# Kernel optimization log

Hardware: AMD Instinct MI355X
Metric: run time of the kernel (lower is better)

The kernel has to match this reference:

```python
import jax, jax.numpy as jnp
import numpy as np

N_NODES = 50000
N_EDGES = 800000
IN_DIM = 128
HID = 128
TIME = 6.0
STEPS = 12


def setup_inputs() -> dict:
    key = jax.random.key(0)
    ks = jax.random.split(key, 8)
    gat_out = jax.random.normal(ks[0], (N_NODES, IN_DIM), dtype=jnp.float32)
    edge_index = jax.random.randint(ks[1], (2, N_EDGES), 0, N_NODES, dtype=jnp.int64)
    # scale weights like PyTorch Linear default (uniform-ish magnitude)
    W_in = jax.random.normal(ks[2], (IN_DIM, HID), dtype=jnp.float32) * (1.0 / np.sqrt(IN_DIM))
    b_in = jnp.zeros((HID,), dtype=jnp.float32)
    W1 = jax.random.normal(ks[3], (HID, 2 * HID), dtype=jnp.float32) * (1.0 / np.sqrt(HID))
    b1 = jnp.zeros((2 * HID,), dtype=jnp.float32)
    W2 = jax.random.normal(ks[4], (2 * HID, HID), dtype=jnp.float32) * (1.0 / np.sqrt(2 * HID))
    b2 = jnp.zeros((HID,), dtype=jnp.float32)
    clearance = jnp.full((1,), 0.1, dtype=jnp.float32)
    return {"gat_out": gat_out, "edge_index": edge_index, "W_in": W_in, "b_in": b_in,
            "W1": W1, "b1": b1, "W2": W2, "b2": b2, "clearance": clearance}


def reference(gat_out, edge_index, W_in, b_in, W1, b1, W2, b2, clearance):
    N = gat_out.shape[0]
    dt = TIME / STEPS
    src, dst = edge_index[0], edge_index[1]
    h = jnp.tanh(gat_out @ W_in + b_in)  # [N, HID]
    # degree is identical each Euler step in the original; hoist it once
    deg = jax.ops.segment_sum(jnp.ones((src.shape[0],), dtype=h.dtype), dst, num_segments=N)
    deg = jnp.clip(deg, 1.0, None)[:, None]  # [N, 1]
    decay = jax.nn.relu(clearance)  # [1]

    def step(h, _):
        agg = jax.ops.segment_sum(h[src], dst, num_segments=N) / deg  # [N, HID]
        diff = jnp.tanh(jax.nn.gelu(agg @ W1 + b1, approximate=False) @ W2 + b2)
        h = h + (diff - decay * h) * dt
        return h, None

    h, _ = jax.lax.scan(step, h, None, length=STEPS)
    return h
```

## Files before the change

kernel.cpp:

```cpp
#include <hip/hip_runtime.h>
#include <math.h>

#define N_NODES 50000
#define N_EDGES 800000
#define HID 128
#define H2 256
#define STEPS 12
#define DT 0.5f

#define NB ((N_NODES + 255) / 256)
#define NODE_BLOCKS ((N_NODES + 31) / 32)
#define N_PAD (NODE_BLOCKS * 32)
#define CSR_CAP (N_EDGES + 8 * N_NODES)

typedef __attribute__((ext_vector_type(8))) short bf16x8;
typedef __attribute__((ext_vector_type(4))) float f32x4;

__device__ inline unsigned short f2bf(float x) {
    unsigned int u = __float_as_uint(x);
    unsigned int r = (u + 0x7FFFu + ((u >> 16) & 1u)) >> 16;
    return (unsigned short)r;
}
__device__ inline float bf2f(unsigned short b) {
    return __uint_as_float(((unsigned int)b) << 16);
}
__device__ inline float u2f(unsigned int u) { return __uint_as_float(u); }

__device__ inline float fast_tanh(float x) {
    float xc = fminf(fmaxf(x, -9.0f), 9.0f);
    float t = __builtin_amdgcn_exp2f(xc * 2.8853900817779268f);
    return 1.0f - 2.0f * __builtin_amdgcn_rcpf(t + 1.0f);
}

__device__ inline float fast_gelu(float x) {
    float u  = x * 0.70710678118654752f;
    float au = fabsf(u);
    float t  = __builtin_amdgcn_rcpf(fmaf(0.3275911f, au, 1.0f));
    float poly = t * (0.254829592f + t * (-0.284496736f + t * (1.421413741f +
                 t * (-1.453152027f + t * 1.061405429f))));
    float ex = __builtin_amdgcn_exp2f(-au * au * 1.4426950408889634f);
    float erfv = copysignf(1.0f - poly * ex, u);
    return 0.5f * x * (1.0f + erfv);
}


__global__ void k_init(int* __restrict__ counts, int* __restrict__ gcur,
                       unsigned short* __restrict__ a, unsigned short* __restrict__ b,
                       const float* __restrict__ W1, const float* __restrict__ W2,
                       const float* __restrict__ Win,
                       unsigned short* __restrict__ w1h, unsigned short* __restrict__ w2h,
                       unsigned short* __restrict__ winh) {
    int i = blockIdx.x * 256 + threadIdx.x;
    if (i == 0) *gcur = 0;
    if (i < N_NODES) counts[i] = 0;
    if (i < (N_PAD - N_NODES) * HID) {
        a[(size_t)N_NODES * HID + i] = 0;
        b[(size_t)N_NODES * HID + i] = 0;
    }
    int tile = i >> 6, l = i & 63;
    if (tile < 160) {
        const float* W; unsigned short* out; int K, N, ti;
        if (tile < 64)       { W = W1;  out = w1h;  K = 128; N = 256; ti = tile; }
        else if (tile < 128) { W = W2;  out = w2h;  K = 256; N = 128; ti = tile - 64; }
        else                 { W = Win; out = winh; K = 128; N = 128; ti = tile - 128; }
        int KT = K >> 5;
        int kt = ti % KT, nt = ti / KT;
        int n  = nt * 16 + (l & 15);
        int k0 = kt * 32 + (l >> 4) * 8;
        int base = ((nt * KT + kt) * 64 + l) * 8;
        for (int j = 0; j < 8; j++)
            out[base + j] = f2bf(W[(size_t)(k0 + j) * N + n]);
    }
}

__global__ void k_hist(const int* __restrict__ dst, int* __restrict__ counts) {
    int e = blockIdx.x * 256 + threadIdx.x;
    if (e < N_EDGES) atomicAdd(&counts[dst[e]], 1);
}

__global__ void k_offsets_atomic(const int* __restrict__ counts, int* __restrict__ gcur,
                                 int* __restrict__ offsets, int* __restrict__ cursor,
                                 int* __restrict__ csr_src) {
    int i = blockIdx.x * 256 + threadIdx.x;
    if (i < N_NODES) {
        int d = counts[i];
        int p = (d + 7) & ~7;
        int o = atomicAdd(gcur, p);
        offsets[i] = o;
        cursor[i]  = o;
        for (int j = d; j < p; j++) csr_src[o + j] = N_NODES;
    }
}

__global__ void k_scatter(const int* __restrict__ src, const int* __restrict__ dst,
                          int* __restrict__ cursor, int* __restrict__ csr_src) {
    int e = blockIdx.x * 256 + threadIdx.x;
    if (e < N_EDGES) {
        int d = dst[e];
        int p = atomicAdd(&cursor[d], 1);
        csr_src[p] = src[e];
    }
}


__global__ __launch_bounds__(256, 3) void k_h0_mfma(
    const float* __restrict__ gat,
    const unsigned short* __restrict__ wh,
    const float* __restrict__ b_in, float* __restrict__ h,
    unsigned short* __restrict__ hbf) {
    __shared__ unsigned short Ahi[32][136];
    __shared__ unsigned short Alo[32][136];
    int tid = threadIdx.x;
    int node0 = blockIdx.x * 32;

    for (int idx = tid; idx < 32 * 64; idx += 256) {
        int m = idx >> 6, c = (idx & 63) * 2;
        float2 v;
        if (node0 + m < N_NODES) v = *(const float2*)&gat[(size_t)(node0 + m) * 128 + c];
        else { v.x = 0.f; v.y = 0.f; }
        unsigned short h0 = f2bf(v.x), h1 = f2bf(v.y);
        unsigned short l0 = f2bf(v.x - bf2f(h0)), l1 = f2bf(v.y - bf2f(h1));
        *(unsigned int*)&Ahi[m][c] = (unsigned int)h0 | ((unsigned int)h1 << 16);
        *(unsigned int*)&Alo[m][c] = (unsigned int)l0 | ((unsigned int)l1 << 16);
    }
    __syncthreads();

    int l = tid & 63, wv = tid >> 6;
    int c15 = l & 15, q = l >> 4;
    f32x4 acc[2][2] = {};
#pragma unroll
    for (int kt = 0; kt < 4; kt++) {
        bf16x8 ah[2], al[2];
#pragma unroll
        for (int mt = 0; mt < 2; mt++) {
            ah[mt] = *(const bf16x8*)&Ahi[mt * 16 + c15][kt * 32 + q * 8];
            al[mt] = *(const bf16x8*)&Alo[mt * 16 + c15][kt * 32 + q * 8];
        }
#pragma unroll
        for (int nn = 0; nn < 2; nn++) {
            int nt = wv * 2 + nn;
            bf16x8 bh = *(const bf16x8*)&wh[(size_t)((nt * 4 + kt) * 64 + l) * 8];
#pragma unroll
            for (int mt = 0; mt < 2; mt++) {
                acc[mt][nn] = __builtin_amdgcn_mfma_f32_16x16x32_bf16(ah[mt], bh, acc[mt][nn], 0, 0, 0);
                acc[mt][nn] = __builtin_amdgcn_mfma_f32_16x16x32_bf16(al[mt], bh, acc[mt][nn], 0, 0, 0);
            }
        }
    }
#pragma unroll
    for (int nn = 0; nn < 2; nn++) {
        int col = (wv * 2 + nn) * 16 + c15;
        float bb = b_in[col];
#pragma unroll
        for (int mt = 0; mt < 2; mt++)
#pragma unroll
            for (int r = 0; r < 4; r++) {
                int node = node0 + mt * 16 + q * 4 + r;
                if (node < N_NODES) {
                    float v = fast_tanh(acc[mt][nn][r] + bb);
                    h[(size_t)node * 128 + col]   = v;
                    hbf[(size_t)node * 128 + col] = f2bf(v);
                }
            }
    }
}


#define ACC8(V) \
    a0 += u2f((V).x << 16); a1 += u2f((V).x & 0xFFFF0000u); \
    a2 += u2f((V).y << 16); a3 += u2f((V).y & 0xFFFF0000u); \
    a4 += u2f((V).z << 16); a5 += u2f((V).z & 0xFFFF0000u); \
    a6 += u2f((V).w << 16); a7 += u2f((V).w & 0xFFFF0000u);

__global__ __launch_bounds__(512, 4) void k_step(
    const unsigned short* __restrict__ hbf_in,
    float* __restrict__ h, unsigned short* __restrict__ hbf_out,
    const int* __restrict__ offsets, const int* __restrict__ csr,
    const int* __restrict__ cnt,
    const unsigned short* __restrict__ w1h,
    const float* __restrict__ b1,
    const unsigned short* __restrict__ w2h,
    const float* __restrict__ b2, const float* __restrict__ clr) {
    __shared__ unsigned short Ahi[32][136];
    __shared__ unsigned short Alo[32][136];
    __shared__ unsigned short Y[32][264];
    int tid = threadIdx.x, l = tid & 63, wv = tid >> 6;
    int c15 = l & 15, q = l >> 4;
    int node0 = blockIdx.x * 32;
    int g  = l >> 4;
    int cl = l & 15;

    {
        int m = wv * 4 + g;
        int node = node0 + m;
        float a0 = 0.f, a1 = 0.f, a2 = 0.f, a3 = 0.f;
        float a4 = 0.f, a5 = 0.f, a6 = 0.f, a7 = 0.f;
        int deg = 0;
        if (node < N_NODES) {
            deg = cnt[node];
            int beg = offsets[node];
            int end = beg + ((deg + 7) & ~7);
            const unsigned short* hb = hbf_in + cl * 8;
            if (beg < end) {
                int4 i0 = *(const int4*)&csr[beg];
                int4 i1 = *(const int4*)&csr[beg + 4];
                for (int e = beg; e < end; e += 8) {
                    int enx = (e + 8 < end) ? (e + 8) : e;
                    int4 j0 = *(const int4*)&csr[enx];
                    int4 j1 = *(const int4*)&csr[enx + 4];
                    uint4 w0 = *(const uint4*)&hb[((unsigned)i0.x) << 7];
                    uint4 w1 = *(const uint4*)&hb[((unsigned)i0.y) << 7];
                    uint4 w2 = *(const uint4*)&hb[((unsigned)i0.z) << 7];
                    uint4 w3 = *(const uint4*)&hb[((unsigned)i0.w) << 7];
                    uint4 w4 = *(const uint4*)&hb[((unsigned)i1.x) << 7];
                    uint4 w5 = *(const uint4*)&hb[((unsigned)i1.y) << 7];
                    uint4 w6 = *(const uint4*)&hb[((unsigned)i1.z) << 7];
                    uint4 w7 = *(const uint4*)&hb[((unsigned)i1.w) << 7];
                    i0 = j0; i1 = j1;
                    ACC8(w0); ACC8(w1); ACC8(w2); ACC8(w3);
                    ACC8(w4); ACC8(w5); ACC8(w6); ACC8(w7);
                }
            }
        }
        float inv = (deg > 1) ? 1.0f / (float)deg : 1.0f;
        float x0 = a0 * inv, x1 = a1 * inv, x2 = a2 * inv, x3 = a3 * inv;
        float x4 = a4 * inv, x5 = a5 * inv, x6 = a6 * inv, x7 = a7 * inv;
        unsigned short h0 = f2bf(x0), h1 = f2bf(x1), h2 = f2bf(x2), h3 = f2bf(x3);
        unsigned short h4 = f2bf(x4), h5 = f2bf(x5), h6 = f2bf(x6), h7 = f2bf(x7);
        uint4 ohi;
        ohi.x = (unsigned int)h0 | ((unsigned int)h1 << 16);
        ohi.y = (unsigned int)h2 | ((unsigned int)h3 << 16);
        ohi.z = (unsigned int)h4 | ((unsigned int)h5 << 16);
        ohi.w = (unsigned int)h6 | ((unsigned int)h7 << 16);
        *(uint4*)&Ahi[m][cl * 8] = ohi;
        unsigned short l0 = f2bf(x0 - bf2f(h0)), l1 = f2bf(x1 - bf2f(h1));
        unsigned short l2 = f2bf(x2 - bf2f(h2)), l3 = f2bf(x3 - bf2f(h3));
        unsigned short l4 = f2bf(x4 - bf2f(h4)), l5 = f2bf(x5 - bf2f(h5));
        unsigned short l6 = f2bf(x6 - bf2f(h6)), l7 = f2bf(x7 - bf2f(h7));
        uint4 olo;
        olo.x = (unsigned int)l0 | ((unsigned int)l1 << 16);
        olo.y = (unsigned int)l2 | ((unsigned int)l3 << 16);
        olo.z = (unsigned int)l4 | ((unsigned int)l5 << 16);
        olo.w = (unsigned int)l6 | ((unsigned int)l7 << 16);
        *(uint4*)&Alo[m][cl * 8] = olo;
    }
    __syncthreads();

    {
        f32x4 acc1[2][2] = {};
#pragma unroll
        for (int kt = 0; kt < 4; kt++) {
            bf16x8 ah[2], al[2];
#pragma unroll
            for (int mt = 0; mt < 2; mt++) {
                ah[mt] = *(const bf16x8*)&Ahi[mt * 16 + c15][kt * 32 + q * 8];
                al[mt] = *(const bf16x8*)&Alo[mt * 16 + c15][kt * 32 + q * 8];
            }
#pragma unroll
            for (int nn = 0; nn < 2; nn++) {
                int nt = wv * 2 + nn;
                bf16x8 bh = *(const bf16x8*)&w1h[(size_t)((nt * 4 + kt) * 64 + l) * 8];
#pragma unroll
                for (int mt = 0; mt < 2; mt++) {
                    acc1[mt][nn] = __builtin_amdgcn_mfma_f32_16x16x32_bf16(ah[mt], bh, acc1[mt][nn], 0, 0, 0);
                    acc1[mt][nn] = __builtin_amdgcn_mfma_f32_16x16x32_bf16(al[mt], bh, acc1[mt][nn], 0, 0, 0);
                }
            }
        }
#pragma unroll
        for (int nn = 0; nn < 2; nn++) {
            int col = (wv * 2 + nn) * 16 + c15;
            float bb = b1[col];
#pragma unroll
            for (int mt = 0; mt < 2; mt++)
#pragma unroll
                for (int r = 0; r < 4; r++) {
                    int row = mt * 16 + q * 4 + r;
                    float x = acc1[mt][nn][r] + bb;
                    Y[row][col] = f2bf(fast_gelu(x));
                }
        }
    }
    __syncthreads();

    f32x4 acc2[2] = {};
#pragma unroll
    for (int kt = 0; kt < 8; kt++) {
        bf16x8 ya[2];
#pragma unroll
        for (int mt = 0; mt < 2; mt++)
            ya[mt] = *(const bf16x8*)&Y[mt * 16 + c15][kt * 32 + q * 8];
        bf16x8 bh = *(const bf16x8*)&w2h[(size_t)((wv * 8 + kt) * 64 + l) * 8];
#pragma unroll
        for (int mt = 0; mt < 2; mt++)
            acc2[mt] = __builtin_amdgcn_mfma_f32_16x16x32_bf16(ya[mt], bh, acc2[mt], 0, 0, 0);
    }
    float decay = fmaxf(clr[0], 0.0f);
    {
        int col = wv * 16 + c15;
        float bb = b2[col];
#pragma unroll
        for (int mt = 0; mt < 2; mt++)
#pragma unroll
            for (int r = 0; r < 4; r++) {
                int node = node0 + mt * 16 + q * 4 + r;
                if (node < N_NODES) {
                    float hv = h[(size_t)node * 128 + col];
                    float diff = fast_tanh(acc2[mt][r] + bb);
                    float nh = hv + (diff - decay * hv) * DT;
                    h[(size_t)node * 128 + col]       = nh;
                    hbf_out[(size_t)node * 128 + col] = f2bf(nh);
                }
            }
    }
}


extern "C" void kernel_launch(void* const* d_in, const int* in_sizes, int n_in,
                              void* d_out, int out_size, void* d_ws, size_t ws_size,
                              hipStream_t stream) {
    const float* gat   = (const float*)d_in[0];
    const int*   edges = (const int*)d_in[1];
    const float* W_in  = (const float*)d_in[2];
    const float* b_in  = (const float*)d_in[3];
    const float* W1    = (const float*)d_in[4];
    const float* b1    = (const float*)d_in[5];
    const float* W2    = (const float*)d_in[6];
    const float* b2    = (const float*)d_in[7];
    const float* clr   = (const float*)d_in[8];
    float* h = (float*)d_out;

    const int* src = edges;
    const int* dst = edges + N_EDGES;

    char* ws = (char*)d_ws;
    size_t off = 0;
    auto alloc = [&](size_t bytes) -> void* {
        off = (off + 255) & ~(size_t)255;
        void* p = ws + off;
        off += bytes;
        return p;
    };
    int*   counts  = (int*)alloc(sizeof(int) * N_NODES);
    int*   offsets = (int*)alloc(sizeof(int) * N_NODES);
    int*   cursor  = (int*)alloc(sizeof(int) * N_NODES);
    int*   gcur    = (int*)alloc(sizeof(int));
    int*   csr_src = (int*)alloc(sizeof(int) * CSR_CAP);
    unsigned short* hbfA = (unsigned short*)alloc(sizeof(short) * (size_t)N_PAD * HID);
    unsigned short* hbfB = (unsigned short*)alloc(sizeof(short) * (size_t)N_PAD * HID);
    unsigned short* w1h  = (unsigned short*)alloc(sizeof(short) * HID * H2);
    unsigned short* w2h  = (unsigned short*)alloc(sizeof(short) * H2 * HID);
    unsigned short* winh = (unsigned short*)alloc(sizeof(short) * HID * HID);

    k_init<<<NB, 256, 0, stream>>>(counts, gcur, hbfA, hbfB,
                                   W1, W2, W_in, w1h, w2h, winh);
    k_hist<<<(N_EDGES + 255) / 256, 256, 0, stream>>>(dst, counts);
    k_offsets_atomic<<<NB, 256, 0, stream>>>(counts, gcur, offsets, cursor, csr_src);
    k_scatter<<<(N_EDGES + 255) / 256, 256, 0, stream>>>(src, dst, cursor, csr_src);

    k_h0_mfma<<<NODE_BLOCKS, 256, 0, stream>>>(gat, winh, b_in, h, hbfA);

    for (int s = 0; s < STEPS; s++) {
        const unsigned short* in = (s & 1) ? hbfB : hbfA;
        unsigned short*      out = (s & 1) ? hbfA : hbfB;
        k_step<<<NODE_BLOCKS, 512, 0, stream>>>(in, h, out, offsets, csr_src, counts,
                                                w1h, b1, w2h, b2, clr);
    }
}
```

Before: 770.8 us.

## Double k_step block to 1024 threads, splitting edges and MFMA tiles across waves

Raises the step kernel from 512 to 1024 threads per 32-node block. Each node's edge list is now split between two 16-lane groups that process alternating 8-edge chunks, and the partial sums are combined with a cross-lane shuffle. The two groups then divide the hi/lo bf16 split writes between them. The two GEMMs are repartitioned so each of the 16 waves owns one output tile, which doubles the parallelism available to hide gather latency. In exchange, launch_bounds(1024,8) tightens register limits, and when degree is small one of the two groups sits idle.

After: 829.9 us. 1.08x slower.

```diff
diff --git a/kernel.cpp b/kernel.cpp
--- a/kernel.cpp
+++ b/kernel.cpp
@@ -172,7 +172,7 @@
     a4 += u2f((V).z << 16); a5 += u2f((V).z & 0xFFFF0000u); \
     a6 += u2f((V).w << 16); a7 += u2f((V).w & 0xFFFF0000u);
 
-__global__ __launch_bounds__(512, 4) void k_step(
+__global__ __launch_bounds__(1024, 8) void k_step(
     const unsigned short* __restrict__ hbf_in,
     float* __restrict__ h, unsigned short* __restrict__ hbf_out,
     const int* __restrict__ offsets, const int* __restrict__ csr,
@@ -191,7 +191,9 @@
     int cl = l & 15;
 
     {
-        int m = wv * 4 + g;
+        int gg = wv * 4 + g;
+        int m  = gg >> 1;
+        int p  = gg & 1;
         int node = node0 + m;
         float a0 = 0.f, a1 = 0.f, a2 = 0.f, a3 = 0.f;
         float a4 = 0.f, a5 = 0.f, a6 = 0.f, a7 = 0.f;
@@ -201,11 +203,12 @@
             int beg = offsets[node];
             int end = beg + ((deg + 7) & ~7);
             const unsigned short* hb = hbf_in + cl * 8;
-            if (beg < end) {
-                int4 i0 = *(const int4*)&csr[beg];
-                int4 i1 = *(const int4*)&csr[beg + 4];
-                for (int e = beg; e < end; e += 8) {
-                    int enx = (e + 8 < end) ? (e + 8) : e;
+            int e = beg + p * 8;
+            if (e < end) {
+                int4 i0 = *(const int4*)&csr[e];
+                int4 i1 = *(const int4*)&csr[e + 4];
+                for (; e < end; e += 16) {
+                    int enx = (e + 16 < end) ? (e + 16) : e;
                     int4 j0 = *(const int4*)&csr[enx];
                     int4 j1 = *(const int4*)&csr[enx + 4];
                     uint4 w0 = *(const uint4*)&hb[((unsigned)i0.x) << 7];
@@ -222,32 +225,40 @@
                 }
             }
         }
+        a0 += __shfl_xor(a0, 16); a1 += __shfl_xor(a1, 16);
+        a2 += __shfl_xor(a2, 16); a3 += __shfl_xor(a3, 16);
+        a4 += __shfl_xor(a4, 16); a5 += __shfl_xor(a5, 16);
+        a6 += __shfl_xor(a6, 16); a7 += __shfl_xor(a7, 16);
+
         float inv = (deg > 1) ? 1.0f / (float)deg : 1.0f;
         float x0 = a0 * inv, x1 = a1 * inv, x2 = a2 * inv, x3 = a3 * inv;
         float x4 = a4 * inv, x5 = a5 * inv, x6 = a6 * inv, x7 = a7 * inv;
         unsigned short h0 = f2bf(x0), h1 = f2bf(x1), h2 = f2bf(x2), h3 = f2bf(x3);
         unsigned short h4 = f2bf(x4), h5 = f2bf(x5), h6 = f2bf(x6), h7 = f2bf(x7);
-        uint4 ohi;
-        ohi.x = (unsigned int)h0 | ((unsigned int)h1 << 16);
-        ohi.y = (unsigned int)h2 | ((unsigned int)h3 << 16);
-        ohi.z = (unsigned int)h4 | ((unsigned int)h5 << 16);
-        ohi.w = (unsigned int)h6 | ((unsigned int)h7 << 16);
-        *(uint4*)&Ahi[m][cl * 8] = ohi;
-        unsigned short l0 = f2bf(x0 - bf2f(h0)), l1 = f2bf(x1 - bf2f(h1));
-        unsigned short l2 = f2bf(x2 - bf2f(h2)), l3 = f2bf(x3 - bf2f(h3));
-        unsigned short l4 = f2bf(x4 - bf2f(h4)), l5 = f2bf(x5 - bf2f(h5));
-        unsigned short l6 = f2bf(x6 - bf2f(h6)), l7 = f2bf(x7 - bf2f(h7));
-        uint4 olo;
-        olo.x = (unsigned int)l0 | ((unsigned int)l1 << 16);
-        olo.y = (unsigned int)l2 | ((unsigned int)l3 << 16);
-        olo.z = (unsigned int)l4 | ((unsigned int)l5 << 16);
-        olo.w = (unsigned int)l6 | ((unsigned int)l7 << 16);
-        *(uint4*)&Alo[m][cl * 8] = olo;
+        if (p == 0) {
+            uint4 o;
+            o.x = (unsigned int)h0 | ((unsigned int)h1 << 16);
+            o.y = (unsigned int)h2 | ((unsigned int)h3 << 16);
+            o.z = (unsigned int)h4 | ((unsigned int)h5 << 16);
+            o.w = (unsigned int)h6 | ((unsigned int)h7 << 16);
+            *(uint4*)&Ahi[m][cl * 8] = o;
+        } else {
+            unsigned short l0 = f2bf(x0 - bf2f(h0)), l1 = f2bf(x1 - bf2f(h1));
+            unsigned short l2 = f2bf(x2 - bf2f(h2)), l3 = f2bf(x3 - bf2f(h3));
+            unsigned short l4 = f2bf(x4 - bf2f(h4)), l5 = f2bf(x5 - bf2f(h5));
+            unsigned short l6 = f2bf(x6 - bf2f(h6)), l7 = f2bf(x7 - bf2f(h7));
+            uint4 o;
+            o.x = (unsigned int)l0 | ((unsigned int)l1 << 16);
+            o.y = (unsigned int)l2 | ((unsigned int)l3 << 16);
+            o.z = (unsigned int)l4 | ((unsigned int)l5 << 16);
+            o.w = (unsigned int)l6 | ((unsigned int)l7 << 16);
+            *(uint4*)&Alo[m][cl * 8] = o;
+        }
     }
     __syncthreads();
 
     {
-        f32x4 acc1[2][2] = {};
+        f32x4 acc1[2] = {};
 #pragma unroll
         for (int kt = 0; kt < 4; kt++) {
             bf16x8 ah[2], al[2];
@@ -256,62 +267,49 @@
                 ah[mt] = *(const bf16x8*)&Ahi[mt * 16 + c15][kt * 32 + q * 8];
                 al[mt] = *(const bf16x8*)&Alo[mt * 16 + c15][kt * 32 + q * 8];
             }
-#pragma unroll
-            for (int nn = 0; nn < 2; nn++) {
-                int nt = wv * 2 + nn;
-                bf16x8 bh = *(const bf16x8*)&w1h[(size_t)((nt * 4 + kt) * 64 + l) * 8];
-#pragma unroll
-                for (int mt = 0; mt < 2; mt++) {
-                    acc1[mt][nn] = __builtin_amdgcn_mfma_f32_16x16x32_bf16(ah[mt], bh, acc1[mt][nn], 0, 0, 0);
-                    acc1[mt][nn] = __builtin_amdgcn_mfma_f32_16x16x32_bf16(al[mt], bh, acc1[mt][nn], 0, 0, 0);
-                }
-            }
-        }
-#pragma unroll
-        for (int nn = 0; nn < 2; nn++) {
-            int col = (wv * 2 + nn) * 16 + c15;
-            float bb = b1[col];
-#pragma unroll
-            for (int mt = 0; mt < 2; mt++)
-#pragma unroll
-                for (int r = 0; r < 4; r++) {
-                    int row = mt * 16 + q * 4 + r;
-                    float x = acc1[mt][nn][r] + bb;
-                    Y[row][col] = f2bf(fast_gelu(x));
-                }
-        }
+            bf16x8 bh = *(const bf16x8*)&w1h[(size_t)((wv * 4 + kt) * 64 + l) * 8];
+#pragma unroll
+            for (int mt = 0; mt < 2; mt++) {
+                acc1[mt] = __builtin_amdgcn_mfma_f32_16x16x32_bf16(ah[mt], bh, acc1[mt], 0, 0, 0);
+                acc1[mt] = __builtin_amdgcn_mfma_f32_16x16x32_bf16(al[mt], bh, acc1[mt], 0, 0, 0);
+            }
+        }
+        int col = wv * 16 + c15;
+        float bb = b1[col];
+#pragma unroll
+        for (int mt = 0; mt < 2; mt++)
+#pragma unroll
+            for (int r = 0; r < 4; r++) {
+                int row = mt * 16 + q * 4 + r;
+                float x = acc1[mt][r] + bb;
+                Y[row][col] = f2bf(fast_gelu(x));
+            }
     }
     __syncthreads();
 
-    f32x4 acc2[2] = {};
-#pragma unroll
-    for (int kt = 0; kt < 8; kt++) {
-        bf16x8 ya[2];
-#pragma unroll
-        for (int mt = 0; mt < 2; mt++)
-            ya[mt] = *(const bf16x8*)&Y[mt * 16 + c15][kt * 32 + q * 8];
-        bf16x8 bh = *(const bf16x8*)&w2h[(size_t)((wv * 8 + kt) * 64 + l) * 8];
-#pragma unroll
-        for (int mt = 0; mt < 2; mt++)
-            acc2[mt] = __builtin_amdgcn_mfma_f32_16x16x32_bf16(ya[mt], bh, acc2[mt], 0, 0, 0);
-    }
-    float decay = fmaxf(clr[0], 0.0f);
     {
-        int col = wv * 16 + c15;
+        int nt2 = wv >> 1, mt2 = wv & 1;
+        f32x4 acc2 = {};
+#pragma unroll
+        for (int kt = 0; kt < 8; kt++) {
+            bf16x8 ya = *(const bf16x8*)&Y[mt2 * 16 + c15][kt * 32 + q * 8];
+            bf16x8 bh = *(const bf16x8*)&w2h[(size_t)((nt2 * 8 + kt) * 64 + l) * 8];
+            acc2 = __builtin_amdgcn_mfma_f32_16x16x32_bf16(ya, bh, acc2, 0, 0, 0);
+        }
+        float decay = fmaxf(clr[0], 0.0f);
+        int col = nt2 * 16 + c15;
         float bb = b2[col];
 #pragma unroll
-        for (int mt = 0; mt < 2; mt++)
-#pragma unroll
-            for (int r = 0; r < 4; r++) {
-                int node = node0 + mt * 16 + q * 4 + r;
-                if (node < N_NODES) {
-                    float hv = h[(size_t)node * 128 + col];
-                    float diff = fast_tanh(acc2[mt][r] + bb);
-                    float nh = hv + (diff - decay * hv) * DT;
-                    h[(size_t)node * 128 + col]       = nh;
-                    hbf_out[(size_t)node * 128 + col] = f2bf(nh);
-                }
-            }
+        for (int r = 0; r < 4; r++) {
+            int node = node0 + mt2 * 16 + q * 4 + r;
+            if (node < N_NODES) {
+                float hv = h[(size_t)node * 128 + col];
+                float diff = fast_tanh(acc2[r] + bb);
+                float nh = hv + (diff - decay * hv) * DT;
+                h[(size_t)node * 128 + col]       = nh;
+                hbf_out[(size_t)node * 128 + col] = f2bf(nh);
+            }
+        }
     }
 }
 
@@ -363,7 +361,7 @@
     for (int s = 0; s < STEPS; s++) {
         const unsigned short* in = (s & 1) ? hbfB : hbfA;
         unsigned short*      out = (s & 1) ? hbfA : hbfB;
-        k_step<<<NODE_BLOCKS, 512, 0, stream>>>(in, h, out, offsets, csr_src, counts,
-                                                w1h, b1, w2h, b2, clr);
-    }
-}
+        k_step<<<NODE_BLOCKS, 1024, 0, stream>>>(in, h, out, offsets, csr_src, counts,
+                                                 w1h, b1, w2h, b2, clr);
+    }
+}
```
